# Kernel optimization log

Hardware: AMD Instinct MI355X
Metric: run time of the kernel (lower is better)

## Reference

```python
import jax, jax.numpy as jnp
import numpy as np

P_LEN, Q_LEN, BATCH, D, H = 300, 50, 32, 256, 256


def _make_params(key):
    ks = jax.random.split(key, 6)
    s = lambda k, shape, fan: jax.random.normal(k, shape, jnp.float32) * (1.0 / np.sqrt(fan))
    return dict(
        Wq=s(ks[0], (2, H, D), D), bq=jnp.zeros((2, H), jnp.float32),
        Wp=s(ks[1], (2, H, D), D), bp=jnp.zeros((2, H), jnp.float32),
        Wr=s(ks[2], (2, H, H), H), br=jnp.zeros((2, H), jnp.float32),
        Wg=s(ks[3], (2, H), H), bg=jnp.zeros((2,), jnp.float32),
        ln_g=jnp.ones((2, 2 * D), jnp.float32), ln_b=jnp.zeros((2, 2 * D), jnp.float32),
        W_ih=s(ks[4], (2, 4 * H, 2 * D), 2 * D), W_hh=s(ks[5], (2, 4 * H, H), H),
        b_ih=jnp.zeros((2, 4 * H), jnp.float32), b_hh=jnp.zeros((2, 4 * H), jnp.float32),
    )


def setup_inputs() -> dict:
    key = jax.random.key(0)
    k1, k2, k3, k4, kp = jax.random.split(key, 5)
    content_vec = jax.random.normal(k1, (P_LEN, BATCH, D), jnp.float32)
    question_vec = jax.random.normal(k2, (Q_LEN, BATCH, D), jnp.float32)
    p_len = jax.random.randint(k3, (BATCH,), P_LEN // 2, P_LEN + 1)
    q_len = jax.random.randint(k4, (BATCH,), Q_LEN // 2, Q_LEN + 1)
    content_mask = (jnp.arange(P_LEN)[None, :] < p_len[:, None]).astype(jnp.int32)
    question_mask = (jnp.arange(Q_LEN)[None, :] < q_len[:, None]).astype(jnp.int32)
    inp = dict(content_vec=content_vec, content_mask=content_mask,
               question_vec=question_vec, question_mask=question_mask)
    inp.update(_make_params(kp))
    return inp


def _masked_flip(v, mask):
    # v: (P, B, D); mask: (B, P). Reverses the valid prefix of each sequence,
    # leaving padding positions in place (standard Match-LSTM masked_flip).
    P = v.shape[0]
    lengths = mask.sum(axis=1)  # (B,)
    t = jnp.arange(P)[:, None]  # (P, 1)
    idx = jnp.where(t < lengths[None, :], lengths[None, :] - 1 - t, t)  # (P, B)
    idx = jnp.broadcast_to(idx[:, :, None], v.shape)
    return jnp.take_along_axis(v, idx, axis=0)


def _uni_match(cv, qv, qmask, Wq, bq, Wp, bp, Wr, br, Wg, bg, ln_g, ln_b, W_ih, W_hh, b_ih, b_hh):
    # cv: (P, B, D), qv: (Q, B, D), qmask: (B, Q)
    B = cv.shape[1]
    Hh = Wr.shape[0]
    wh = jnp.einsum('qbd,hd->qbh', qv, Wq) + bq      # (Q, B, H), precomputed once
    hp_all = jnp.einsum('pbd,hd->pbh', cv, Wp) + bp  # (P, B, H), precomputed
    pad = (qmask == 0)                               # (B, Q)

    def step(carry, xs):
        h, c = carry
        cv_t, hp_t = xs
        hr = h @ Wr.T + br                                    # (B, H)
        g = jnp.tanh(wh + hp_t[None] + hr[None])              # (Q, B, H)
        alpha = (jnp.einsum('qbh,h->qb', g, Wg) + bg).T       # (B, Q)
        alpha = jax.nn.softmax(jnp.where(pad, -jnp.inf, alpha), axis=1)
        h_alpha = jnp.einsum('bq,qbd->bd', alpha, qv)         # (B, D)
        z = jnp.concatenate([cv_t, h_alpha], axis=1)          # (B, 2D)
        mu = jnp.mean(z, axis=-1, keepdims=True)
        var = jnp.mean((z - mu) ** 2, axis=-1, keepdims=True)
        z = (z - mu) * jax.lax.rsqrt(var + 1e-5) * ln_g + ln_b
        gates = z @ W_ih.T + b_ih + h @ W_hh.T + b_hh         # (B, 4H)
        i_, f_, g_, o_ = jnp.split(gates, 4, axis=1)          # torch LSTMCell order i,f,g,o
        c_n = jax.nn.sigmoid(f_) * c + jax.nn.sigmoid(i_) * jnp.tanh(g_)
        h_n = jax.nn.sigmoid(o_) * jnp.tanh(c_n)
        return (h_n, c_n), h_n

    h0 = jnp.zeros((B, Hh), cv.dtype)
    _, hs = jax.lax.scan(step, (h0, h0), (cv, hp_all))
    return hs  # (P, B, H)


def reference(content_vec, content_mask, question_vec, question_mask,
              Wq, bq, Wp, bp, Wr, br, Wg, bg, ln_g, ln_b, W_ih, W_hh, b_ih, b_hh):
    # Dropout with p=0 (inference) is identity.
    args = lambda i: (Wq[i], bq[i], Wp[i], bp[i], Wr[i], br[i], Wg[i], bg[i],
                      ln_g[i], ln_b[i], W_ih[i], W_hh[i], b_ih[i], b_hh[i])
    right = _uni_match(content_vec, question_vec, question_mask, *args(0))
    cv_flip = _masked_flip(content_vec, content_mask)
    left = _uni_match(cv_flip, question_vec, question_mask, *args(1))
    left = _masked_flip(left, content_mask)
    res = jnp.concatenate([right, left], axis=2)            # (P, B, 2H)
    return content_mask.T[:, :, None].astype(res.dtype) * res
```

## Files before the change

kernel.cpp:

```cpp
#include <hip/hip_runtime.h>
#include <hip/hip_fp16.h>

typedef unsigned int u32;
typedef unsigned long long u64;
typedef _Float16 half2_t __attribute__((ext_vector_type(2)));

static constexpr int PL = 300;
static constexpr int QL = 50;
static constexpr int B  = 32;
static constexpr int D  = 256;
static constexpr int H  = 256;

__device__ __forceinline__ float fdot2(u32 w, u32 x, float acc) {
    return __builtin_amdgcn_fdot2(__builtin_bit_cast(half2_t, w),
                                  __builtin_bit_cast(half2_t, x), acc, false);
}
__device__ __forceinline__ u32 packh2(float a, float b) {
    half2_t h2; h2[0] = (_Float16)a; h2[1] = (_Float16)b;
    return __builtin_bit_cast(u32, h2);
}

__global__ __launch_bounds__(256) void pack_whh(const float* __restrict__ Whh,
                                                u32* __restrict__ dst) {
    int id = blockIdx.x * 256 + threadIdx.x;
    int dd = id >> 17;
    int r  = id & 131071;
    int kc = r >> 12;
    int R  = (r >> 2) & 1023;
    int w  = r & 3;
    int k  = kc * 8 + w * 2;
    const float* s = &Whh[((size_t)dd * 1024 + R) * 256 + k];
    dst[id] = packh2(s[0], s[1]);
}

__global__ __launch_bounds__(256) void pack_wr8(const float* __restrict__ W,
                                                u32* __restrict__ dst) {
    int id = blockIdx.x * 256 + threadIdx.x;
    int g  = id >> 15;
    int r  = id & 32767;
    int kc = r >> 10;
    int c  = (r >> 2) & 255;
    int w  = r & 3;
    int k  = kc * 8 + w * 2;
    const float* s = &W[(g * 256 + c) * 256 + k];
    dst[id] = packh2(s[0], s[1]);
}

__global__ __launch_bounds__(256) void prep_proj(const float* __restrict__ X,
                                                 const float* __restrict__ W,
                                                 const float* __restrict__ Bv,
                                                 __half* __restrict__ out,
                                                 int T, int nt) {
    int id = blockIdx.x;
    int tb = id % nt; id /= nt;
    int b  = id % B;  id /= B;
    int g  = id;
    int t0 = tb * 8;
    int nr = T - t0; if (nr > 8) nr = 8;
    __shared__ __align__(16) float xs[8][256];
    int tid = threadIdx.x;
    for (int r = 0; r < nr; r++) xs[r][tid] = X[((t0 + r) * B + b) * D + tid];
    __syncthreads();
    const float4* wrow = (const float4*)&W[(g * H + tid) * D];
    float bb = Bv[g * H + tid];
    float acc[8];
#pragma unroll
    for (int r = 0; r < 8; r++) acc[r] = bb;
    for (int d4 = 0; d4 < D / 4; d4++) {
        float4 w = wrow[d4];
#pragma unroll
        for (int r = 0; r < 8; r++) {
            float4 x = *(const float4*)&xs[r][d4 * 4];
            acc[r] = fmaf(w.x, x.x, fmaf(w.y, x.y, fmaf(w.z, x.z, fmaf(w.w, x.w, acc[r]))));
        }
    }
    for (int r = 0; r < nr; r++)
        out[((g * B + b) * T + t0 + r) * H + tid] = __float2half(acc[r]);
}

__global__ __launch_bounds__(256) void p1_prep(const float* __restrict__ cv,
                                               const float* __restrict__ Wih,
                                               const float* __restrict__ lng,
                                               __half* __restrict__ P1) {
    int id = blockIdx.x;
    int tb = id % 38; id /= 38;
    int b  = id % 32; id /= 32;
    int dd = id;
    int t0 = tb * 8;
    int nr = PL - t0; if (nr > 8) nr = 8;
    __shared__ __align__(16) float xs[8][256];
    int tid = threadIdx.x;
    float g = lng[dd * 512 + tid];
    for (int r = 0; r < nr; r++)
        xs[r][tid] = cv[((size_t)(t0 + r) * B + b) * D + tid] * g;
    __syncthreads();
    for (int gc = 0; gc < 4; gc++) {
        int R = gc * 256 + tid;
        const float4* wrow = (const float4*)&Wih[((size_t)dd * 1024 + R) * 512];
        float acc[8] = {};
        for (int d4 = 0; d4 < 64; d4++) {
            float4 w = wrow[d4];
#pragma unroll
            for (int r = 0; r < 8; r++) {
                float4 x = *(const float4*)&xs[r][d4 * 4];
                acc[r] = fmaf(w.x, x.x, fmaf(w.y, x.y, fmaf(w.z, x.z, fmaf(w.w, x.w, acc[r]))));
            }
        }
        for (int r = 0; r < nr; r++)
            P1[((size_t)(dd * 32 + b) * PL + t0 + r) * 1024 + R] = __float2half(acc[r]);
    }
}

__global__ __launch_bounds__(256) void vp_prep(const float* __restrict__ qv,
                                               const float* __restrict__ Wih,
                                               const float* __restrict__ lng,
                                               __half* __restrict__ VP) {
    int blk = blockIdx.x;
    int dd = blk >> 8, b = (blk >> 3) & 31, rc = blk & 7;
    __shared__ __align__(16) u32 qg[50 * 128];
    __shared__ __align__(16) u32 wch[128 * 128];
    int tid = threadIdx.x;
    for (int v = tid; v < 6400; v += 256) {
        int q = v >> 7, i = v & 127;
        float a = qv[((size_t)q * 32 + b) * 256 + 2 * i]     * lng[dd * 512 + 256 + 2 * i];
        float c = qv[((size_t)q * 32 + b) * 256 + 2 * i + 1] * lng[dd * 512 + 256 + 2 * i + 1];
        qg[v] = packh2(a, c);
    }
    for (int v = tid; v < 16384; v += 256) {
        int rl = v >> 7, i = v & 127;
        int r = rc * 128 + rl;
        float a = Wih[((size_t)dd * 1024 + r) * 512 + 256 + 2 * i];
        float c = Wih[((size_t)dd * 1024 + r) * 512 + 256 + 2 * i + 1];
        wch[v] = packh2(a, c);
    }
    __syncthreads();
    for (int p = tid; p < 128 * 56; p += 256) {
        int rl = p / 56, q = p % 56;
        int r = rc * 128 + rl;
        float acc = 0.f;
        if (q < 50) {
            const u32* qr = qg + q * 128;
            const u32* wr = wch + rl * 128;
#pragma unroll 8
            for (int i = 0; i < 128; i++) acc = fdot2(wr[i], qr[i], acc);
        }
        VP[((size_t)(dd * 32 + b) * 1024 + r) * 56 + q] = __float2half(acc);
    }
}

__global__ __launch_bounds__(256) void gram_prep(const float* __restrict__ qv,
                                                 float* __restrict__ G,
                                                 float* __restrict__ qs) {
    int b = blockIdx.x;
    __shared__ float qvs[50 * 256];
    int tid = threadIdx.x;
    for (int v = tid; v < 12800; v += 256) {
        int q = v >> 8, k = v & 255;
        qvs[v] = qv[((size_t)q * 32 + b) * 256 + k];
    }
    __syncthreads();
    for (int p = tid; p < 2500; p += 256) {
        int q = p / 50, q2 = p % 50;
        float acc = 0.f;
        for (int k = 0; k < 256; k++) acc = fmaf(qvs[q * 256 + k], qvs[q2 * 256 + k], acc);
        G[((size_t)b * 50 + q) * 50 + q2] = acc;
    }
    if (tid < 52) {
        float s = 0.f;
        if (tid < 50) for (int k = 0; k < 256; k++) s += qvs[tid * 256 + k];
        qs[b * 52 + tid] = s;
    }
}

__global__ __launch_bounds__(256) void cvstats_prep(const float* __restrict__ cv,
                                                    float* __restrict__ st) {
    int blk = blockIdx.x;
    int t = blk >> 5, b = blk & 31;
    int tid = threadIdx.x;
    float v = cv[((size_t)t * 32 + b) * 256 + tid];
    float s = v, s2 = v * v;
#pragma unroll
    for (int m = 32; m; m >>= 1) { s += __shfl_xor(s, m, 64); s2 += __shfl_xor(s2, m, 64); }
    __shared__ float red[8];
    if ((tid & 63) == 0) { red[(tid >> 6) * 2] = s; red[(tid >> 6) * 2 + 1] = s2; }
    __syncthreads();
    if (tid == 0) {
        float S = red[0] + red[2] + red[4] + red[6];
        float S2 = red[1] + red[3] + red[5] + red[7];
        st[((size_t)b * 300 + t) * 2] = S;
        st[((size_t)b * 300 + t) * 2 + 1] = S2;
    }
}

__global__ __launch_bounds__(256) void c1c2_prep(const float* __restrict__ Wih,
                                                 const float* __restrict__ lng,
                                                 const float* __restrict__ lnb,
                                                 const float* __restrict__ bih,
                                                 const float* __restrict__ bhh,
                                                 float* __restrict__ C12) {
    int id = blockIdx.x * 256 + threadIdx.x;
    int dd = id >> 10, R = id & 1023;
    float s1 = 0.f, s2 = 0.f;
    const float* wr = &Wih[((size_t)dd * 1024 + R) * 512];
    for (int k = 0; k < 512; k++) {
        float w = wr[k];
        s1 = fmaf(w, lng[dd * 512 + k], s1);
        s2 = fmaf(w, lnb[dd * 512 + k], s2);
    }
    C12[(size_t)id * 2] = s1;
    C12[(size_t)id * 2 + 1] = s2 + bih[dd * 1024 + R] + bhh[dd * 1024 + R];
}

__global__ __launch_bounds__(1024, 1) void scan13(
    const int*   __restrict__ cmask,
    const int*   __restrict__ qmask,
    const float* __restrict__ Wgv,
    const float* __restrict__ bgv,
    const float* __restrict__ brp,
    const u32*   __restrict__ WhhP,
    const u32*   __restrict__ WrP,
    const __half* __restrict__ whp,
    const __half* __restrict__ hpp,
    const __half* __restrict__ P1,
    const __half* __restrict__ VP,
    const float* __restrict__ C12,
    const float* __restrict__ G,
    const float* __restrict__ qsr,
    const float* __restrict__ cvst,
    float* __restrict__ out)
{
    int blk = blockIdx.x;
    int dd = blk >> 5, j = blk & 31;
    int tid = threadIdx.x;
    int lane = tid & 63, wave = tid >> 6;

    __shared__ __align__(16) u32 sh_wh[6400];
    __shared__ float sh_G[50 * 50];
    __shared__ __align__(16) u32 sh_h[128];
    __shared__ float sh_a[256];
    __shared__ float sh_gk[1024];
    __shared__ float sh_af[64];
    __shared__ __align__(16) u32 sh_al2[28];
    __shared__ float sh_alpha[64];
    __shared__ float sh_qb[64];
    __shared__ float sh_qs[52];
    __shared__ float sh_r2[4];
    __shared__ float sh_cs[2];
    __shared__ int   sh_len1;

    {
        const u32* whsrc = (const u32*)(whp + (size_t)(dd * 32 + j) * QL * H);
        for (int i = tid; i < 6400; i += 1024) sh_wh[i] = whsrc[i];
    }
    for (int v = tid; v < 2500; v += 1024) sh_G[v] = G[(size_t)j * 2500 + v];
    if (tid < 52) sh_qs[tid] = qsr[j * 52 + tid];
    if (tid >= 64 && tid < 128) {
        int q = tid - 64;
        sh_qb[q] = (q < QL) ? (qmask[j * QL + q] ? 0.f : -1e30f) : -1e30f;
    }
    if (tid >= 128 && tid < 256) sh_h[tid - 128] = 0;
    if (tid == 0) sh_len1 = 0;
    __syncthreads();
    {
        int s = 0;
        for (int tt = tid; tt < PL; tt += 1024) s += cmask[j * PL + tt];
#pragma unroll
        for (int m = 32; m; m >>= 1) s += __shfl_xor(s, m, 64);
        if (lane == 0) atomicAdd(&sh_len1, s);
    }
    __syncthreads();
    int len_j = sh_len1;

    float wgr[4];
#pragma unroll
    for (int i = 0; i < 4; i++) wgr[i] = Wgv[dd * H + lane + 64 * i];
    float bgs = bgv[dd];
    float brv = (tid < 256) ? brp[dd * H + tid] : 0.f;
    float C1r = C12[((size_t)dd * 1024 + tid) * 2];
    float C2r = C12[((size_t)dd * 1024 + tid) * 2 + 1];
    float c_reg = 0.f;

    if (tid < 256)
        for (int t = len_j; t < PL; t++)
            out[((size_t)t * B + j) * 512 + dd * 256 + tid] = 0.f;

    const __half* hpb = hpp + (size_t)(dd * 32 + j) * PL * H;
    const u32* VPu = (const u32*)VP;
    const uint4* whq = (const uint4*)WhhP + (size_t)dd * 32 * 1024;
    const uint4* wrq = (const uint4*)WrP  + (size_t)dd * 32 * 256;
    bool ishr = (tid < 256);

    for (int t = 0; t < len_j; t++) {
        int tsj = dd ? (len_j - 1 - t) : t;
        __syncthreads();

        float p1v = __half2float(P1[((size_t)(dd * 32 + j) * PL + tsj) * 1024 + tid]);
        float hpv = ishr ? __half2float(hpb[(size_t)tsj * H + tid]) : 0.f;
        if (tid == 0) {
            sh_cs[0] = cvst[((size_t)j * 300 + tsj) * 2];
            sh_cs[1] = cvst[((size_t)j * 300 + tsj) * 2 + 1];
        }
        uint4 vp[7];
        {
            const uint4* vr = (const uint4*)(VPu + ((size_t)(dd * 32 + j) * 1024 + tid) * 28);
#pragma unroll
            for (int i = 0; i < 7; i++) vp[i] = vr[i];
        }

        float g0 = 0.f, hr = 0.f;
#pragma unroll 8
        for (int kc = 0; kc < 32; kc++) {
            uint4 hx = *(const uint4*)(sh_h + kc * 4);
            uint4 wa = whq[kc * 1024 + tid];
            g0 = fdot2(wa.x, hx.x, g0); g0 = fdot2(wa.y, hx.y, g0);
            g0 = fdot2(wa.z, hx.z, g0); g0 = fdot2(wa.w, hx.w, g0);
            if (ishr) {
                uint4 wr = wrq[kc * 256 + tid];
                hr = fdot2(wr.x, hx.x, hr); hr = fdot2(wr.y, hx.y, hr);
                hr = fdot2(wr.z, hx.z, hr); hr = fdot2(wr.w, hx.w, hr);
            }
        }
        if (ishr) sh_a[tid] = hr + brv + hpv;
        __syncthreads();

        {
            float av[4];
#pragma unroll
            for (int i = 0; i < 4; i++) av[i] = sh_a[lane + 64 * i];
            const __half* wh16 = (const __half*)sh_wh;
            for (int q = wave; q < QL; q += 16) {
                float a = 0.f;
#pragma unroll
                for (int i = 0; i < 4; i++) {
                    float xx = (float)wh16[q * 256 + lane + 64 * i] + av[i];
                    float e = __expf(2.f * xx);
                    a = fmaf(wgr[i], (e - 1.f) / (e + 1.f), a);
                }
#pragma unroll
                for (int m = 32; m; m >>= 1) a += __shfl_xor(a, m, 64);
                if (lane == 0) sh_alpha[q] = a + bgs + sh_qb[q];
            }
        }
        __syncthreads();

        if (wave == 0) {
            float v = (lane < QL) ? sh_alpha[lane] : -1e30f;
            float m = v;
#pragma unroll
            for (int s = 32; s; s >>= 1) m = fmaxf(m, __shfl_xor(m, s, 64));
            float e = (lane < QL) ? __expf(v - m) : 0.f;
            float sum = e;
#pragma unroll
            for (int s = 32; s; s >>= 1) sum += __shfl_xor(sum, s, 64);
            float al = (lane < QL) ? e / sum : 0.f;
            sh_af[lane] = al;
            float alo = __shfl_xor(al, 1, 64);
            if (!(lane & 1) && lane < 56) sh_al2[lane >> 1] = packh2(al, alo);
        }
        __syncthreads();

        if (wave == 0) {
            float gd = 0.f;
            if (lane < QL) {
                const float* Grow = sh_G + lane * 50;
                float aq = sh_af[lane];
                for (int q2 = 0; q2 < QL; q2++) gd = fmaf(Grow[q2], sh_af[q2], gd);
                gd *= aq;
            }
#pragma unroll
            for (int m = 32; m; m >>= 1) gd += __shfl_xor(gd, m, 64);
            if (lane == 0) sh_r2[0] = gd;
        } else if (wave == 1) {
            float s = (lane < QL) ? sh_af[lane] * sh_qs[lane] : 0.f;
#pragma unroll
            for (int m = 32; m; m >>= 1) s += __shfl_xor(s, m, 64);
            if (lane == 0) sh_r2[1] = s;
        }
        __syncthreads();

        {
            float acc = 0.f;
#pragma unroll
            for (int i = 0; i < 7; i++) {
                acc = fdot2(vp[i].x, sh_al2[i * 4 + 0], acc);
                acc = fdot2(vp[i].y, sh_al2[i * 4 + 1], acc);
                acc = fdot2(vp[i].z, sh_al2[i * 4 + 2], acc);
                acc = fdot2(vp[i].w, sh_al2[i * 4 + 3], acc);
            }
            float mu = (sh_cs[0] + sh_r2[1]) * (1.f / 512.f);
            float E2 = (sh_cs[1] + sh_r2[0]) * (1.f / 512.f);
            float rs = rsqrtf(E2 - mu * mu + 1e-5f);
            sh_gk[tid] = g0 + rs * (p1v + acc) - rs * mu * C1r + C2r;
        }
        __syncthreads();

        if (ishr) {
            float gi = sh_gk[tid], gf = sh_gk[256 + tid];
            float gg = sh_gk[512 + tid], go = sh_gk[768 + tid];
            float si = 1.f / (1.f + __expf(-gi));
            float sf = 1.f / (1.f + __expf(-gf));
            float so = 1.f / (1.f + __expf(-go));
            float eg = __expf(2.f * gg); float tg = (eg - 1.f) / (eg + 1.f);
            float c = sf * c_reg + si * tg;
            float ec = __expf(2.f * c); float tc = (ec - 1.f) / (ec + 1.f);
            float hv = so * tc;
            c_reg = c;
            float ho = __shfl_xor(hv, 1, 64);
            if (!(tid & 1)) sh_h[tid >> 1] = packh2(hv, ho);
            out[((size_t)tsj * B + j) * 512 + dd * 256 + tid] = hv;
        }
    }
}

extern "C" void kernel_launch(void* const* d_in, const int* in_sizes, int n_in,
                              void* d_out, int out_size, void* d_ws, size_t ws_size,
                              hipStream_t stream) {
    const float* cv    = (const float*)d_in[0];
    const int*   cmask = (const int*)  d_in[1];
    const float* qv    = (const float*)d_in[2];
    const int*   qmask = (const int*)  d_in[3];
    const float* Wq    = (const float*)d_in[4];
    const float* bq    = (const float*)d_in[5];
    const float* Wp    = (const float*)d_in[6];
    const float* bp    = (const float*)d_in[7];
    const float* Wr    = (const float*)d_in[8];
    const float* br    = (const float*)d_in[9];
    const float* Wg    = (const float*)d_in[10];
    const float* bg    = (const float*)d_in[11];
    const float* ln_g  = (const float*)d_in[12];
    const float* ln_b  = (const float*)d_in[13];
    const float* Wih   = (const float*)d_in[14];
    const float* Whh   = (const float*)d_in[15];
    const float* b_ih  = (const float*)d_in[16];
    const float* b_hh  = (const float*)d_in[17];
    float* out = (float*)d_out;

    uint8_t* ws = (uint8_t*)d_ws;
    u32*    WhhP = (u32*)ws;     ws += (size_t)2 * 32 * 1024 * 4 * 4;
    u32*    WrP  = (u32*)ws;     ws += (size_t)2 * 32 * 256 * 4 * 4;
    __half* VP  = (__half*)ws;   ws += (size_t)2 * 32 * 1024 * 56 * 2;
    __half* whp = (__half*)ws;   ws += (size_t)2 * 32 * 50 * 256 * 2;
    __half* hpp = (__half*)ws;   ws += (size_t)2 * 32 * 300 * 256 * 2;
    __half* P1  = (__half*)ws;   ws += (size_t)2 * 32 * 300 * 1024 * 2;
    float*  C12 = (float*)ws;    ws += (size_t)2 * 1024 * 2 * 4;
    float*  G   = (float*)ws;    ws += (size_t)32 * 50 * 50 * 4;
    float*  qs  = (float*)ws;    ws += (size_t)32 * 52 * 4;
    float*  cvs = (float*)ws;

    hipLaunchKernelGGL(pack_whh, dim3(1024), dim3(256), 0, stream, Whh, WhhP);
    hipLaunchKernelGGL(pack_wr8, dim3(256), dim3(256), 0, stream, Wr, WrP);
    hipLaunchKernelGGL(prep_proj, dim3(2 * 32 * 7), dim3(256), 0, stream,
                       qv, Wq, bq, whp, QL, 7);
    hipLaunchKernelGGL(prep_proj, dim3(2 * 32 * 38), dim3(256), 0, stream,
                       cv, Wp, bp, hpp, PL, 38);
    hipLaunchKernelGGL(p1_prep, dim3(2 * 32 * 38), dim3(256), 0, stream,
                       cv, Wih, ln_g, P1);
    hipLaunchKernelGGL(vp_prep, dim3(512), dim3(256), 0, stream, qv, Wih, ln_g, VP);
    hipLaunchKernelGGL(gram_prep, dim3(32), dim3(256), 0, stream, qv, G, qs);
    hipLaunchKernelGGL(cvstats_prep, dim3(9600), dim3(256), 0, stream, cv, cvs);
    hipLaunchKernelGGL(c1c2_prep, dim3(8), dim3(256), 0, stream,
                       Wih, ln_g, ln_b, b_ih, b_hh, C12);
    hipLaunchKernelGGL(scan13, dim3(64), dim3(1024), 0, stream,
                       cmask, qmask, Wg, bg, br, WhhP, WrP, whp, hpp, P1, VP, C12, G, qs, cvs,
                       out);
}
```

Measured before the change: 4.142 ms.

## Replace block barriers with LDS counter flags and specialize waves per stage

Replaces the per-step __syncthreads barriers in the recurrent scan with workgroup-scope atomic counters in LDS. Only the waves that need a result wait for it, so the gate matvec in the other waves overlaps the attention and softmax work of waves 0-3. Rows 832-1023 of the packed W_hh are cached in LDS to cut global weight traffic, and the loop-invariant VP register loads and cvstats loads are hoisted or made per-thread. The costs are spin-wait polling, a much larger LDS footprint, and subtler ordering correctness between waves.

```diff
diff --git a/kernel.cpp b/kernel.cpp
--- a/kernel.cpp
+++ b/kernel.cpp
@@ -2,7 +2,6 @@
 #include <hip/hip_fp16.h>
 
 typedef unsigned int u32;
-typedef unsigned long long u64;
 typedef _Float16 half2_t __attribute__((ext_vector_type(2)));
 
 static constexpr int PL = 300;
@@ -18,6 +17,13 @@
 __device__ __forceinline__ u32 packh2(float a, float b) {
     half2_t h2; h2[0] = (_Float16)a; h2[1] = (_Float16)b;
     return __builtin_bit_cast(u32, h2);
+}
+__device__ __forceinline__ void spin_lds(u32* c, u32 want) {
+    while (__hip_atomic_load(c, __ATOMIC_ACQUIRE, __HIP_MEMORY_SCOPE_WORKGROUP) < want)
+        __builtin_amdgcn_s_sleep(1);
+}
+__device__ __forceinline__ void pub_lds(u32* c) {
+    __hip_atomic_fetch_add(c, 1u, __ATOMIC_RELEASE, __HIP_MEMORY_SCOPE_WORKGROUP);
 }
 
 __global__ __launch_bounds__(256) void pack_whh(const float* __restrict__ Whh,
@@ -211,7 +217,7 @@
     C12[(size_t)id * 2 + 1] = s2 + bih[dd * 1024 + R] + bhh[dd * 1024 + R];
 }
 
-__global__ __launch_bounds__(1024, 1) void scan13(
+__global__ __launch_bounds__(1024, 1) void scan14(
     const int*   __restrict__ cmask,
     const int*   __restrict__ qmask,
     const float* __restrict__ Wgv,
@@ -234,8 +240,9 @@
     int tid = threadIdx.x;
     int lane = tid & 63, wave = tid >> 6;
 
+    __shared__ __align__(16) u32 sh_whL[192 * 132];
     __shared__ __align__(16) u32 sh_wh[6400];
-    __shared__ float sh_G[50 * 50];
+    __shared__ float sh_G[2500];
     __shared__ __align__(16) u32 sh_h[128];
     __shared__ float sh_a[256];
     __shared__ float sh_gk[1024];
@@ -244,10 +251,17 @@
     __shared__ float sh_alpha[64];
     __shared__ float sh_qb[64];
     __shared__ float sh_qs[52];
-    __shared__ float sh_r2[4];
-    __shared__ float sh_cs[2];
+    __shared__ float sh_r2[2];
     __shared__ int   sh_len1;
-
+    __shared__ u32 cH, cA, cL, cSM, cGK;
+
+    const uint4* whq = (const uint4*)WhhP + (size_t)dd * 32 * 1024;
+    const uint4* wrq = (const uint4*)WrP  + (size_t)dd * 32 * 256;
+
+    for (int v = tid; v < 192 * 32; v += 1024) {
+        int r = v >> 5, kc = v & 31;
+        *(uint4*)&sh_whL[r * 132 + kc * 4] = whq[kc * 1024 + 832 + r];
+    }
     {
         const u32* whsrc = (const u32*)(whp + (size_t)(dd * 32 + j) * QL * H);
         for (int i = tid; i < 6400; i += 1024) sh_wh[i] = whsrc[i];
@@ -259,7 +273,7 @@
         sh_qb[q] = (q < QL) ? (qmask[j * QL + q] ? 0.f : -1e30f) : -1e30f;
     }
     if (tid >= 128 && tid < 256) sh_h[tid - 128] = 0;
-    if (tid == 0) sh_len1 = 0;
+    if (tid == 0) { sh_len1 = 0; cH = 4; cA = 0; cL = 0; cSM = 0; cGK = 0; }
     __syncthreads();
     {
         int s = 0;
@@ -278,6 +292,12 @@
     float brv = (tid < 256) ? brp[dd * H + tid] : 0.f;
     float C1r = C12[((size_t)dd * 1024 + tid) * 2];
     float C2r = C12[((size_t)dd * 1024 + tid) * 2 + 1];
+    uint4 vp[7];
+    {
+        const uint4* vr = (const uint4*)((const u32*)VP + ((size_t)(dd * 32 + j) * 1024 + tid) * 28);
+#pragma unroll
+        for (int i = 0; i < 7; i++) vp[i] = vr[i];
+    }
     float c_reg = 0.f;
 
     if (tid < 256)
@@ -285,99 +305,105 @@
             out[((size_t)t * B + j) * 512 + dd * 256 + tid] = 0.f;
 
     const __half* hpb = hpp + (size_t)(dd * 32 + j) * PL * H;
-    const u32* VPu = (const u32*)VP;
-    const uint4* whq = (const uint4*)WhhP + (size_t)dd * 32 * 1024;
-    const uint4* wrq = (const uint4*)WrP  + (size_t)dd * 32 * 256;
-    bool ishr = (tid < 256);
+    bool isA = (tid < 256);
+    int rL = tid - 832;
 
     for (int t = 0; t < len_j; t++) {
+        u32 w4 = 4u * (t + 1);
         int tsj = dd ? (len_j - 1 - t) : t;
-        __syncthreads();
+        spin_lds(&cH, w4);
 
         float p1v = __half2float(P1[((size_t)(dd * 32 + j) * PL + tsj) * 1024 + tid]);
-        float hpv = ishr ? __half2float(hpb[(size_t)tsj * H + tid]) : 0.f;
-        if (tid == 0) {
-            sh_cs[0] = cvst[((size_t)j * 300 + tsj) * 2];
-            sh_cs[1] = cvst[((size_t)j * 300 + tsj) * 2 + 1];
-        }
-        uint4 vp[7];
-        {
-            const uint4* vr = (const uint4*)(VPu + ((size_t)(dd * 32 + j) * 1024 + tid) * 28);
-#pragma unroll
-            for (int i = 0; i < 7; i++) vp[i] = vr[i];
-        }
-
-        float g0 = 0.f, hr = 0.f;
+        float cs0 = cvst[((size_t)j * 300 + tsj) * 2];
+        float cs1 = cvst[((size_t)j * 300 + tsj) * 2 + 1];
+        float g0 = 0.f;
+
+        if (isA) {
+            float hpv = __half2float(hpb[(size_t)tsj * H + tid]);
+            float hr = 0.f;
 #pragma unroll 8
-        for (int kc = 0; kc < 32; kc++) {
-            uint4 hx = *(const uint4*)(sh_h + kc * 4);
-            uint4 wa = whq[kc * 1024 + tid];
-            g0 = fdot2(wa.x, hx.x, g0); g0 = fdot2(wa.y, hx.y, g0);
-            g0 = fdot2(wa.z, hx.z, g0); g0 = fdot2(wa.w, hx.w, g0);
-            if (ishr) {
-                uint4 wr = wrq[kc * 256 + tid];
-                hr = fdot2(wr.x, hx.x, hr); hr = fdot2(wr.y, hx.y, hr);
-                hr = fdot2(wr.z, hx.z, hr); hr = fdot2(wr.w, hx.w, hr);
-            }
-        }
-        if (ishr) sh_a[tid] = hr + brv + hpv;
-        __syncthreads();
-
-        {
-            float av[4];
-#pragma unroll
-            for (int i = 0; i < 4; i++) av[i] = sh_a[lane + 64 * i];
-            const __half* wh16 = (const __half*)sh_wh;
-            for (int q = wave; q < QL; q += 16) {
-                float a = 0.f;
-#pragma unroll
-                for (int i = 0; i < 4; i++) {
-                    float xx = (float)wh16[q * 256 + lane + 64 * i] + av[i];
-                    float e = __expf(2.f * xx);
-                    a = fmaf(wgr[i], (e - 1.f) / (e + 1.f), a);
+            for (int kc = 0; kc < 32; kc++) {
+                uint4 hx = *(const uint4*)(sh_h + kc * 4);
+                uint4 w = wrq[kc * 256 + tid];
+                hr = fdot2(w.x, hx.x, hr); hr = fdot2(w.y, hx.y, hr);
+                hr = fdot2(w.z, hx.z, hr); hr = fdot2(w.w, hx.w, hr);
+            }
+            sh_a[tid] = hr + brv + hpv;
+            if (lane == 0) pub_lds(&cA);
+#pragma unroll 8
+            for (int kc = 0; kc < 32; kc++) {
+                uint4 hx = *(const uint4*)(sh_h + kc * 4);
+                uint4 wa = whq[kc * 1024 + tid];
+                g0 = fdot2(wa.x, hx.x, g0); g0 = fdot2(wa.y, hx.y, g0);
+                g0 = fdot2(wa.z, hx.z, g0); g0 = fdot2(wa.w, hx.w, g0);
+            }
+            spin_lds(&cA, w4);
+            {
+                float av[4];
+#pragma unroll
+                for (int i = 0; i < 4; i++) av[i] = sh_a[lane + 64 * i];
+                const __half* wh16 = (const __half*)sh_wh;
+                for (int q = wave; q < QL; q += 4) {
+                    float a = 0.f;
+#pragma unroll
+                    for (int i = 0; i < 4; i++) {
+                        float xx = (float)wh16[q * 256 + lane + 64 * i] + av[i];
+                        float e = __expf(2.f * xx);
+                        a = fmaf(wgr[i], (e - 1.f) / (e + 1.f), a);
+                    }
+#pragma unroll
+                    for (int m = 32; m; m >>= 1) a += __shfl_xor(a, m, 64);
+                    if (lane == 0) sh_alpha[q] = a + bgs + sh_qb[q];
                 }
-#pragma unroll
-                for (int m = 32; m; m >>= 1) a += __shfl_xor(a, m, 64);
-                if (lane == 0) sh_alpha[q] = a + bgs + sh_qb[q];
-            }
-        }
-        __syncthreads();
-
-        if (wave == 0) {
-            float v = (lane < QL) ? sh_alpha[lane] : -1e30f;
-            float m = v;
-#pragma unroll
-            for (int s = 32; s; s >>= 1) m = fmaxf(m, __shfl_xor(m, s, 64));
-            float e = (lane < QL) ? __expf(v - m) : 0.f;
-            float sum = e;
-#pragma unroll
-            for (int s = 32; s; s >>= 1) sum += __shfl_xor(sum, s, 64);
-            float al = (lane < QL) ? e / sum : 0.f;
-            sh_af[lane] = al;
-            float alo = __shfl_xor(al, 1, 64);
-            if (!(lane & 1) && lane < 56) sh_al2[lane >> 1] = packh2(al, alo);
-        }
-        __syncthreads();
-
-        if (wave == 0) {
-            float gd = 0.f;
-            if (lane < QL) {
-                const float* Grow = sh_G + lane * 50;
-                float aq = sh_af[lane];
-                for (int q2 = 0; q2 < QL; q2++) gd = fmaf(Grow[q2], sh_af[q2], gd);
-                gd *= aq;
-            }
-#pragma unroll
-            for (int m = 32; m; m >>= 1) gd += __shfl_xor(gd, m, 64);
-            if (lane == 0) sh_r2[0] = gd;
-        } else if (wave == 1) {
-            float s = (lane < QL) ? sh_af[lane] * sh_qs[lane] : 0.f;
-#pragma unroll
-            for (int m = 32; m; m >>= 1) s += __shfl_xor(s, m, 64);
-            if (lane == 0) sh_r2[1] = s;
-        }
-        __syncthreads();
-
+            }
+            if (lane == 0) pub_lds(&cL);
+            if (wave == 0) {
+                spin_lds(&cL, w4);
+                float v = (lane < QL) ? sh_alpha[lane] : -1e30f;
+                float m = v;
+#pragma unroll
+                for (int s = 32; s; s >>= 1) m = fmaxf(m, __shfl_xor(m, s, 64));
+                float e = (lane < QL) ? __expf(v - m) : 0.f;
+                float sum = e;
+#pragma unroll
+                for (int s = 32; s; s >>= 1) sum += __shfl_xor(sum, s, 64);
+                float al = (lane < QL) ? e / sum : 0.f;
+                sh_af[lane] = al;
+                float alo = __shfl_xor(al, 1, 64);
+                if (!(lane & 1) && lane < 56) sh_al2[lane >> 1] = packh2(al, alo);
+                float gd = 0.f;
+                if (lane < QL) {
+                    const float* Grow = sh_G + lane * 50;
+                    for (int q2 = 0; q2 < QL; q2++) gd = fmaf(Grow[q2], sh_af[q2], gd);
+                    gd *= al;
+                }
+                float qd = (lane < QL) ? al * sh_qs[lane] : 0.f;
+#pragma unroll
+                for (int s = 32; s; s >>= 1) {
+                    gd += __shfl_xor(gd, s, 64); qd += __shfl_xor(qd, s, 64);
+                }
+                if (lane == 0) { sh_r2[0] = gd; sh_r2[1] = qd; }
+                if (lane == 0) pub_lds(&cSM);
+            }
+        } else if (rL >= 0) {
+#pragma unroll 8
+            for (int kc = 0; kc < 32; kc++) {
+                uint4 hx = *(const uint4*)(sh_h + kc * 4);
+                uint4 wa = *(const uint4*)&sh_whL[rL * 132 + kc * 4];
+                g0 = fdot2(wa.x, hx.x, g0); g0 = fdot2(wa.y, hx.y, g0);
+                g0 = fdot2(wa.z, hx.z, g0); g0 = fdot2(wa.w, hx.w, g0);
+            }
+        } else {
+#pragma unroll 8
+            for (int kc = 0; kc < 32; kc++) {
+                uint4 hx = *(const uint4*)(sh_h + kc * 4);
+                uint4 wa = whq[kc * 1024 + tid];
+                g0 = fdot2(wa.x, hx.x, g0); g0 = fdot2(wa.y, hx.y, g0);
+                g0 = fdot2(wa.z, hx.z, g0); g0 = fdot2(wa.w, hx.w, g0);
+            }
+        }
+
+        spin_lds(&cSM, (u32)(t + 1));
         {
             float acc = 0.f;
 #pragma unroll
@@ -387,14 +413,15 @@
                 acc = fdot2(vp[i].z, sh_al2[i * 4 + 2], acc);
                 acc = fdot2(vp[i].w, sh_al2[i * 4 + 3], acc);
             }
-            float mu = (sh_cs[0] + sh_r2[1]) * (1.f / 512.f);
-            float E2 = (sh_cs[1] + sh_r2[0]) * (1.f / 512.f);
+            float mu = (cs0 + sh_r2[1]) * (1.f / 512.f);
+            float E2 = (cs1 + sh_r2[0]) * (1.f / 512.f);
             float rs = rsqrtf(E2 - mu * mu + 1e-5f);
             sh_gk[tid] = g0 + rs * (p1v + acc) - rs * mu * C1r + C2r;
         }
-        __syncthreads();
-
-        if (ishr) {
+        if (lane == 0) pub_lds(&cGK);
+
+        if (isA) {
+            spin_lds(&cGK, 16u * (t + 1));
             float gi = sh_gk[tid], gf = sh_gk[256 + tid];
             float gg = sh_gk[512 + tid], go = sh_gk[768 + tid];
             float si = 1.f / (1.f + __expf(-gi));
@@ -408,6 +435,7 @@
             float ho = __shfl_xor(hv, 1, 64);
             if (!(tid & 1)) sh_h[tid >> 1] = packh2(hv, ho);
             out[((size_t)tsj * B + j) * 512 + dd * 256 + tid] = hv;
+            if (lane == 0) pub_lds(&cH);
         }
     }
 }
@@ -460,7 +488,7 @@
     hipLaunchKernelGGL(cvstats_prep, dim3(9600), dim3(256), 0, stream, cv, cvs);
     hipLaunchKernelGGL(c1c2_prep, dim3(8), dim3(256), 0, stream,
                        Wih, ln_g, ln_b, b_ih, b_hh, C12);
-    hipLaunchKernelGGL(scan13, dim3(64), dim3(1024), 0, stream,
+    hipLaunchKernelGGL(scan14, dim3(64), dim3(1024), 0, stream,
                        cmask, qmask, Wg, bg, br, WhhP, WrP, whp, hpp, P1, VP, C12, G, qs, cvs,
                        out);
 }
```

Measured after the change: 5.247 ms. 26.7% more time.
